# Kernel optimization log

Measured on AMD Instinct MI355X. Metric: run time of the kernel, lower is better.

Reference implementation:

```python
import jax, jax.numpy as jnp
import numpy as np

B, C, F, W, H, E = 2, 8, 256, 512, 8, 4
HD = F // H

def mc_linear(x, w):
    # per-channel linear over features: (b,c,f,w) x (c,g,f) -> (b,c,g,w)
    return jnp.einsum('bcfw,cgf->bcgw', x, w)

def conv2d(x, k, b, ph, pw, groups=1):
    y = jax.lax.conv_general_dilated(x, k, (1, 1), ((ph, ph), (pw, pw)),
                                     dimension_numbers=('NCHW', 'OIHW', 'NCHW'),
                                     feature_group_count=groups)
    return y + b[None, :, None, None]

def mc_ln(x, g, b, eps=1e-5):
    # MultichannelLayerNorm: layernorm over features axis (dim 2), per-channel affine
    m = jnp.mean(x, axis=2, keepdims=True)
    v = jnp.var(x, axis=2, keepdims=True)
    return (x - m) * jax.lax.rsqrt(v + eps) * g[None, :, :, None] + b[None, :, :, None]

def sq_relu(x):
    return jnp.square(jax.nn.relu(x))

def rope(x):
    # x: (b,c,H,n,d); interleaved rotary (lucidrains rotary_embedding_torch)
    n, d = x.shape[-2], x.shape[-1]
    inv = 1.0 / (10000.0 ** (jnp.arange(0, d, 2, dtype=jnp.float32) / d))
    fr = jnp.arange(n, dtype=jnp.float32)[:, None] * inv[None, :]
    cos = jnp.repeat(jnp.cos(fr), 2, axis=-1)
    sin = jnp.repeat(jnp.sin(fr), 2, axis=-1)
    x2 = x.reshape(x.shape[:-1] + (d // 2, 2))
    xr = jnp.stack((-x2[..., 1], x2[..., 0]), axis=-1).reshape(x.shape)
    return x * cos + xr * sin

def mc_attn(x, mem, Wq, Kq, bq, Wk, Kk, bk, Wv, Kv, bv, Wo):
    b, c, f, w = x.shape
    def proj(t, Wl, Kc, bc):
        y = conv2d(mc_linear(t, Wl), Kc, bc, 0, 1)               # (b,c,f,w)
        y = y.transpose(0, 1, 3, 2).reshape(b, c, w, H, HD)
        return y.transpose(0, 1, 3, 2, 4)                        # (b,c,H,w,hd)
    q = rope(proj(x, Wq, Kq, bq))
    k = rope(proj(mem, Wk, Kk, bk))
    v = proj(mem, Wv, Kv, bv)
    # NOTE: original divides by sqrt(h) where h == features, not head_dim
    qk = jnp.einsum('bchnd,bchmd->bchnm', q, k) / jnp.sqrt(jnp.float32(f))
    a = jnp.einsum('bchnm,bchmd->bchnd', jax.nn.softmax(qk, axis=-1), v)
    a = a.transpose(0, 1, 3, 2, 4).reshape(b, c, w, f).transpose(0, 1, 3, 2)
    return mc_linear(a, Wo)

def _forward(x, skip, Wq, Kq, bq, Wk, Kk, bk, Wv, Kv, bv, Wo,
             norm_g, norm_b, c1a_w, c1a_b, c1b_w, c1b_b, c2_w, c2_b, w3, w4):
    att = lambda i, t, m: mc_attn(t, m, Wq[i], Kq[i], bq[i], Wk[i], Kk[i], bk[i],
                                  Wv[i], Kv[i], bv[i], Wo[i])
    h = x  # embed is Identity since channels == out_channels; dropout in eval mode
    z = mc_ln(h, norm_g[0], norm_b[0])
    h = h + att(0, z, z) + att(1, z, skip)
    z = mc_ln(h, norm_g[1], norm_b[1])
    za = sq_relu(conv2d(z, c1a_w, c1a_b, 5, 0, groups=C))   # FrameConv k=11 depthwise
    zb = conv2d(z, c1b_w, c1b_b, 3, 0, groups=C)            # FrameConv k=7 depthwise
    z = conv2d(mc_ln(za + zb, norm_g[2], norm_b[2]), c2_w, c2_b, 3, 0, groups=C)
    h = h + z
    z4 = mc_ln(h, norm_g[3], norm_b[3])
    h = h + att(2, z4, z4)
    h = h + att(3, mc_ln(h, norm_g[4], norm_b[4]), skip)
    z = mc_linear(sq_relu(mc_linear(mc_ln(h, norm_g[5], norm_b[5]), w3)), w4)
    h = h + z
    return jnp.concatenate((x, h), axis=1)

def setup_inputs():
    key = jax.random.key(0)
    ks = jax.random.split(key, 16)
    s = 0.02
    r = lambda k, shp: jax.random.normal(k, shp, dtype=jnp.float32) * s
    return dict(
        x=jax.random.normal(ks[0], (B, C, F, W), dtype=jnp.float32),
        skip=jax.random.normal(ks[1], (B, C, F, W), dtype=jnp.float32),
        Wq=r(ks[2], (4, C, F, F)), Kq=r(ks[3], (4, C, C, 1, 3)), bq=jnp.zeros((4, C), jnp.float32),
        Wk=r(ks[4], (4, C, F, F)), Kk=r(ks[5], (4, C, C, 1, 3)), bk=jnp.zeros((4, C), jnp.float32),
        Wv=r(ks[6], (4, C, F, F)), Kv=r(ks[7], (4, C, C, 1, 3)), bv=jnp.zeros((4, C), jnp.float32),
        Wo=r(ks[8], (4, C, F, F)),
        norm_g=jnp.ones((6, C, F), jnp.float32), norm_b=jnp.zeros((6, C, F), jnp.float32),
        c1a_w=r(ks[9], (C, 1, 11, 1)), c1a_b=jnp.zeros((C,), jnp.float32),
        c1b_w=r(ks[10], (C, 1, 7, 1)), c1b_b=jnp.zeros((C,), jnp.float32),
        c2_w=r(ks[11], (C, 1, 7, 1)), c2_b=jnp.zeros((C,), jnp.float32),
        w3=r(ks[12], (C, E, F)), w4=r(ks[13], (C, F, E)),
    )

def reference(x, skip, Wq, Kq, bq, Wk, Kk, bk, Wv, Kv, bv, Wo,
              norm_g, norm_b, c1a_w, c1a_b, c1b_w, c1b_b, c2_w, c2_b, w3, w4):
    return _forward(x, skip, Wq, Kq, bq, Wk, Kk, bk, Wv, Kv, bv, Wo,
                    norm_g, norm_b, c1a_w, c1a_b, c1b_w, c1b_b, c2_w, c2_b, w3, w4)
```

## Files before the change

### kernel.cpp

```cpp
#include <hip/hip_runtime.h>

#define B_ 2
#define C_ 8
#define F_ 256
#define W_ 512
#define H_ 8
#define FW_ (F_*W_)
#define CFW_ (C_*FW_)
#define OBS_ (2*CFW_)

typedef unsigned short u16;

__device__ __forceinline__ u16 f2bf(float f){
  unsigned u = __float_as_uint(f);
  u += 0x7fffu + ((u>>16)&1u);
  return (u16)(u>>16);
}
__device__ __forceinline__ float bf2f(u16 u){
  return __uint_as_float((unsigned)u<<16);
}

typedef __attribute__((ext_vector_type(8))) short bf16x8;
typedef __attribute__((ext_vector_type(4))) float f32x4;

__global__ __launch_bounds__(256)
void init_out(const float* __restrict__ x, float* __restrict__ out){
  int i = blockIdx.x*256 + threadIdx.x;
  int b = i >> 20;
  int r = i & (CFW_-1);
  float v = x[i];
  out[(size_t)b*OBS_ + r] = v;
  out[(size_t)b*OBS_ + CFW_ + r] = v;
}

__global__ void put_val(float* o, float v){ o[0] = v; }

__global__ __launch_bounds__(256)
void cvt5(const float* __restrict__ s0, const float* __restrict__ s1,
          const float* __restrict__ s2, const float* __restrict__ s3,
          const float* __restrict__ s4,
          u16* __restrict__ d0, u16* __restrict__ d1, u16* __restrict__ d2,
          u16* __restrict__ d3, u16* __restrict__ d4){
  int which = blockIdx.y;
  const float* s = which==0 ? s0 : which==1 ? s1 : which==2 ? s2 : which==3 ? s3 : s4;
  u16* d        = which==0 ? d0 : which==1 ? d1 : which==2 ? d2 : which==3 ? d3 : d4;
  int i = (blockIdx.x*256 + threadIdx.x)*4;
  float4 v = *(const float4*)(s + i);
  ushort4 o;
  o.x = f2bf(v.x); o.y = f2bf(v.y); o.z = f2bf(v.z); o.w = f2bf(v.w);
  *(ushort4*)(d + i) = o;
}

template<int BF16OUT>
__global__ __launch_bounds__(256)
void ln32(const float* __restrict__ X, long xbs, void* __restrict__ Yv, long ybs,
          const float* __restrict__ g, const float* __restrict__ bta){
  int wl = threadIdx.x & 31, fs = threadIdx.x >> 5;
  int w = blockIdx.x*32 + wl;
  int c = blockIdx.y;
  int b = blockIdx.z;
  const float* xb = X + (size_t)b*xbs + (size_t)c*FW_ + w;
  float v[32];
  float sum = 0.f, sq = 0.f;
  #pragma unroll
  for (int i = 0; i < 32; ++i){
    v[i] = xb[(size_t)(fs*32 + i)*W_];
    sum += v[i]; sq += v[i]*v[i];
  }
  __shared__ float Ss[8][32], Sq[8][32], Mu[32], Rs[32];
  Ss[fs][wl] = sum; Sq[fs][wl] = sq;
  __syncthreads();
  if (fs == 0){
    float s = 0.f, q = 0.f;
    #pragma unroll
    for (int j = 0; j < 8; ++j){ s += Ss[j][wl]; q += Sq[j][wl]; }
    float mu = s * (1.f/256.f);
    float var = q * (1.f/256.f) - mu*mu;
    Mu[wl] = mu; Rs[wl] = rsqrtf(var + 1e-5f);
  }
  __syncthreads();
  float mu = Mu[wl], rs = Rs[wl];
  if (BF16OUT){
    u16* yb = (u16*)Yv + (size_t)b*ybs + (size_t)c*FW_ + w;
    #pragma unroll
    for (int i = 0; i < 32; ++i){
      int f = fs*32 + i;
      yb[(size_t)f*W_] = f2bf((v[i] - mu)*rs*g[c*F_ + f] + bta[c*F_ + f]);
    }
  } else {
    float* yb = (float*)Yv + (size_t)b*ybs + (size_t)c*FW_ + w;
    #pragma unroll
    for (int i = 0; i < 32; ++i){
      int f = fs*32 + i;
      yb[(size_t)f*W_] = (v[i] - mu)*rs*g[c*F_ + f] + bta[c*F_ + f];
    }
  }
}

__global__ __launch_bounds__(256)
void gemm_qkv_b(const u16* __restrict__ wqb, const u16* __restrict__ wkb,
                const u16* __restrict__ wvb,
                const u16* __restrict__ srcq, const u16* __restrict__ srckv,
                u16* __restrict__ T){
  int zid = blockIdx.z;
  int proj = zid >> 4;
  int bc = zid & 15; int b = bc >> 3, c = bc & 7;
  const u16* src = (proj == 0) ? srcq : srckv;
  const u16* Wm  = (proj == 0) ? wqb : (proj == 1 ? wkb : wvb);
  const u16* Ax = src + (size_t)b*CFW_ + (size_t)c*FW_;
  const u16* Bw = Wm + (size_t)c*F_*F_;
  u16* Yb = T + (size_t)proj*2*CFW_ + (size_t)b*CFW_ + (size_t)c*FW_;

  int w0 = blockIdx.x * 64;
  int g0 = blockIdx.y * 64;
  int t = threadIdx.x, lane = t & 63, wv_ = t >> 6;
  int gq = lane >> 4, c16 = lane & 15;
  int wm = w0 + wv_*16 + c16;
  const f32x4 zero4 = {0.f,0.f,0.f,0.f};
  f32x4 acc[4] = {zero4, zero4, zero4, zero4};

  for (int k0 = 0; k0 < F_; k0 += 32){
    union { bf16x8 v8; u16 u[8]; } af;
    #pragma unroll
    for (int j = 0; j < 8; ++j)
      af.u[j] = Ax[(size_t)(k0 + 8*gq + j)*W_ + wm];
    #pragma unroll
    for (int nf = 0; nf < 4; ++nf){
      bf16x8 bfr = *(const bf16x8*)(Bw + (size_t)(g0 + nf*16 + c16)*F_ + k0 + 8*gq);
      acc[nf] = __builtin_amdgcn_mfma_f32_16x16x32_bf16(af.v8, bfr, acc[nf], 0, 0, 0);
    }
  }
  int wout = w0 + wv_*16 + 4*gq;
  #pragma unroll
  for (int nf = 0; nf < 4; ++nf){
    ushort4 o;
    o.x = f2bf(acc[nf][0]); o.y = f2bf(acc[nf][1]);
    o.z = f2bf(acc[nf][2]); o.w = f2bf(acc[nf][3]);
    *(ushort4*)(Yb + (size_t)(g0 + nf*16 + c16)*W_ + wout) = o;
  }
}

__global__ __launch_bounds__(256)
void gemm_wo_b(const u16* __restrict__ wob, const u16* __restrict__ A,
               float* __restrict__ Y){
  int bc = blockIdx.z; int b = bc >> 3, c = bc & 7;
  const u16* Ax = A + (size_t)b*CFW_ + (size_t)c*FW_;
  const u16* Bw = wob + (size_t)c*F_*F_;
  float* Yb = Y + (size_t)b*OBS_ + (size_t)c*FW_;
  int w0 = blockIdx.x * 64;
  int g0 = blockIdx.y * 64;
  int t = threadIdx.x, lane = t & 63, wv_ = t >> 6;
  int gq = lane >> 4, c16 = lane & 15;
  int wm = w0 + wv_*16 + c16;
  const f32x4 zero4 = {0.f,0.f,0.f,0.f};
  f32x4 acc[4] = {zero4, zero4, zero4, zero4};

  for (int k0 = 0; k0 < F_; k0 += 32){
    union { bf16x8 v8; u16 u[8]; } af;
    #pragma unroll
    for (int j = 0; j < 8; ++j)
      af.u[j] = Ax[(size_t)(k0 + 8*gq + j)*W_ + wm];
    #pragma unroll
    for (int nf = 0; nf < 4; ++nf){
      bf16x8 bfr = *(const bf16x8*)(Bw + (size_t)(g0 + nf*16 + c16)*F_ + k0 + 8*gq);
      acc[nf] = __builtin_amdgcn_mfma_f32_16x16x32_bf16(af.v8, bfr, acc[nf], 0, 0, 0);
    }
  }
  int wout = w0 + wv_*16 + 4*gq;
  #pragma unroll
  for (int nf = 0; nf < 4; ++nf){
    float* y = Yb + (size_t)(g0 + nf*16 + c16)*W_ + wout;
    float4 o = *(float4*)y;
    o.x += acc[nf][0]; o.y += acc[nf][1]; o.z += acc[nf][2]; o.w += acc[nf][3];
    *(float4*)y = o;
  }
}

__global__ __launch_bounds__(256)
void conv_rope_lds(const u16* __restrict__ T,
                   const float* __restrict__ Kq3, const float* __restrict__ bq,
                   const float* __restrict__ Kk3, const float* __restrict__ bk,
                   const float* __restrict__ Kv3, const float* __restrict__ bv,
                   u16* __restrict__ Q, u16* __restrict__ K,
                   u16* __restrict__ V){
  __shared__ float Tin[16][514];
  __shared__ float Kc[192];
  int bx = blockIdx.x;
  int jf = bx & 127;
  int b  = (bx >> 7) & 1;
  int p  = bx >> 8;
  const float* K3   = p==0 ? Kq3 : (p==1 ? Kk3 : Kv3);
  const float* bias = p==0 ? bq  : (p==1 ? bk  : bv);
  const u16* Tb = T + (size_t)p*2*CFW_ + (size_t)b*CFW_;
  u16* O = (p==0 ? Q : (p==1 ? K : V)) + (size_t)b*CFW_;
  int f0 = jf*2;
  int t = threadIdx.x;

  if (t < 192) Kc[t] = K3[t];
  if (t < 16){ Tin[t][0] = 0.f; Tin[t][513] = 0.f; }
  for (int li = t; li < 16*128; li += 256){
    int row = li >> 7;
    int c4  = li & 127;
    int ci = row >> 1, fsel = row & 1;
    ushort4 v4 = *(const ushort4*)(Tb + ((size_t)ci*F_ + f0 + fsel)*W_ + c4*4);
    float* dst = &Tin[row][1 + c4*4];
    dst[0] = bf2f(v4.x); dst[1] = bf2f(v4.y);
    dst[2] = bf2f(v4.z); dst[3] = bf2f(v4.w);
  }
  __syncthreads();

  int co = t >> 5;
  int wg = t & 31;
  int wbase = wg*16;
  float bs = bias[co];
  float a0[16], a1[16];
  #pragma unroll
  for (int i = 0; i < 16; ++i){ a0[i] = bs; a1[i] = bs; }
  #pragma unroll
  for (int ci = 0; ci < 8; ++ci){
    const float* r0 = &Tin[ci*2+0][1 + wbase];
    const float* r1 = &Tin[ci*2+1][1 + wbase];
    float k0 = Kc[(co*8+ci)*3+0], k1 = Kc[(co*8+ci)*3+1], k2 = Kc[(co*8+ci)*3+2];
    #pragma unroll
    for (int i = 0; i < 16; ++i){
      a0[i] += k0*r0[i-1] + k1*r0[i] + k2*r0[i+1];
      a1[i] += k0*r1[i-1] + k1*r1[i] + k2*r1[i+1];
    }
  }
  size_t obase = ((size_t)co*F_ + f0)*W_ + wbase;
  if (p < 2){
    int j = jf & 15;
    float inv = exp2f(-(float)j * 0.83048202372184f);
    float sv, cv, dsn, dcs;
    sincosf((float)wbase * inv, &sv, &cv);
    sincosf(inv, &dsn, &dcs);
    float scale = (p == 0) ? 0.0625f : 1.f;
    u16 o0[16], o1[16];
    #pragma unroll
    for (int i = 0; i < 16; ++i){
      o0[i] = f2bf((a0[i]*cv - a1[i]*sv)*scale);
      o1[i] = f2bf((a1[i]*cv + a0[i]*sv)*scale);
      float cn = cv*dcs - sv*dsn;
      sv = sv*dcs + cv*dsn;
      cv = cn;
    }
    #pragma unroll
    for (int q4 = 0; q4 < 4; ++q4){
      *(ushort4*)(O + obase + q4*4)      = make_ushort4(o0[q4*4],o0[q4*4+1],o0[q4*4+2],o0[q4*4+3]);
      *(ushort4*)(O + obase + W_ + q4*4) = make_ushort4(o1[q4*4],o1[q4*4+1],o1[q4*4+2],o1[q4*4+3]);
    }
  } else {
    #pragma unroll
    for (int q4 = 0; q4 < 4; ++q4){
      ushort4 p0, p1;
      p0.x = f2bf(a0[q4*4+0]); p0.y = f2bf(a0[q4*4+1]);
      p0.z = f2bf(a0[q4*4+2]); p0.w = f2bf(a0[q4*4+3]);
      p1.x = f2bf(a1[q4*4+0]); p1.y = f2bf(a1[q4*4+1]);
      p1.z = f2bf(a1[q4*4+2]); p1.w = f2bf(a1[q4*4+3]);
      *(ushort4*)(O + obase + q4*4)      = p0;
      *(ushort4*)(O + obase + W_ + q4*4) = p1;
    }
  }
}

__global__ __launch_bounds__(512)
void attn_mfma_b(const u16* __restrict__ q, const u16* __restrict__ k,
                 const u16* __restrict__ v, u16* __restrict__ a){
  extern __shared__ __align__(16) unsigned char smem_dyn[];
  u16* ks = (u16*)smem_dyn;
  u16* vs = ks + 512*40;
  u16* ps = vs + 32*520;
  int bx = blockIdx.x;
  int b = bx >> 6;
  int ch = bx & 63;
  int h = ch & 7, c = ch >> 3;
  size_t base = (size_t)b*CFW_ + ((size_t)c*F_ + h*32)*W_;
  int t = threadIdx.x;
  int lane = t & 63, wv = t >> 6;
  int g = lane >> 4, c16 = lane & 15;

  int q0 = blockIdx.y*128 + wv*16;
  union { bf16x8 v8; u16 u[8]; } aq;
  #pragma unroll
  for (int j = 0; j < 8; ++j)
    aq.u[j] = q[base + (size_t)(8*g + j)*W_ + q0 + c16];

  for (int d = 0; d < 32; ++d)
    ks[t*40 + d] = k[base + (size_t)d*W_ + t];
  {
    int m8 = (t & 63)*8;
    #pragma unroll
    for (int it = 0; it < 4; ++it){
      int d = (t >> 6) + it*8;
      *(uint4*)(vs + (size_t)d*520 + m8) = *(const uint4*)(v + base + (size_t)d*W_ + m8);
    }
  }
  __syncthreads();

  u16* pw = ps + (size_t)wv*16*136;

  float mrun[4] = {-3e38f,-3e38f,-3e38f,-3e38f};
  float lrun[4] = {0.f,0.f,0.f,0.f};
  const f32x4 zero4 = {0.f,0.f,0.f,0.f};
  f32x4 outacc[2] = {zero4, zero4};

  for (int kt = 0; kt < 4; ++kt){
    f32x4 sv[8];
    #pragma unroll
    for (int mi = 0; mi < 8; ++mi){
      int m0 = kt*128 + mi*16;
      bf16x8 kb8 = *(const bf16x8*)(ks + (size_t)(m0 + c16)*40 + 8*g);
      sv[mi] = __builtin_amdgcn_mfma_f32_16x16x32_bf16(aq.v8, kb8, zero4, 0, 0, 0);
    }
    float pmax[4];
    #pragma unroll
    for (int r = 0; r < 4; ++r){
      float m = sv[0][r];
      #pragma unroll
      for (int mi = 1; mi < 8; ++mi) m = fmaxf(m, sv[mi][r]);
      pmax[r] = m;
    }
    #pragma unroll
    for (int mask = 1; mask <= 8; mask <<= 1){
      #pragma unroll
      for (int r = 0; r < 4; ++r)
        pmax[r] = fmaxf(pmax[r], __shfl_xor(pmax[r], mask));
    }
    float corr[4];
    #pragma unroll
    for (int r = 0; r < 4; ++r){
      float mn = fmaxf(mrun[r], pmax[r]);
      corr[r] = __expf(mrun[r] - mn);
      mrun[r] = mn;
      lrun[r] *= corr[r];
    }
    #pragma unroll
    for (int mi = 0; mi < 8; ++mi){
      #pragma unroll
      for (int r = 0; r < 4; ++r){
        float p = __expf(sv[mi][r] - mrun[r]);
        lrun[r] += p;
        pw[(size_t)(4*g + r)*136 + mi*16 + c16] = f2bf(p);
      }
    }
    f32x4 cv = {corr[0], corr[1], corr[2], corr[3]};
    outacc[0] *= cv;
    outacc[1] *= cv;
    #pragma unroll
    for (int mc = 0; mc < 4; ++mc){
      bf16x8 pa  = *(const bf16x8*)(pw + (size_t)c16*136 + mc*32 + 8*g);
      bf16x8 vb0 = *(const bf16x8*)(vs + (size_t)c16*520      + kt*128 + mc*32 + 8*g);
      bf16x8 vb1 = *(const bf16x8*)(vs + (size_t)(16+c16)*520 + kt*128 + mc*32 + 8*g);
      outacc[0] = __builtin_amdgcn_mfma_f32_16x16x32_bf16(pa, vb0, outacc[0], 0, 0, 0);
      outacc[1] = __builtin_amdgcn_mfma_f32_16x16x32_bf16(pa, vb1, outacc[1], 0, 0, 0);
    }
  }
  float L[4];
  #pragma unroll
  for (int r = 0; r < 4; ++r){
    float s = lrun[r];
    #pragma unroll
    for (int mask = 1; mask <= 8; mask <<= 1) s += __shfl_xor(s, mask);
    L[r] = s;
  }
  #pragma unroll
  for (int dt = 0; dt < 2; ++dt){
    ushort4 o;
    o.x = f2bf(outacc[dt][0] / L[0]);
    o.y = f2bf(outacc[dt][1] / L[1]);
    o.z = f2bf(outacc[dt][2] / L[2]);
    o.w = f2bf(outacc[dt][3] / L[3]);
    *(ushort4*)(a + base + (size_t)(dt*16 + c16)*W_ + q0 + 4*g) = o;
  }
}

__global__ __launch_bounds__(256)
void dw_fuse_b(const float* __restrict__ Z, long zbs,
               const float* __restrict__ k11, const float* __restrict__ b11,
               const float* __restrict__ k7,  const float* __restrict__ b7,
               float* __restrict__ S, long sbs){
  int w = blockIdx.x*256 + threadIdx.x;
  int f = blockIdx.y;
  int bc = blockIdx.z; int b = bc >> 3, c = bc & 7;
  const float* zb = Z + (size_t)b*zbs + (size_t)c*FW_;
  float a = b11[c];
  #pragma unroll
  for (int i = 0; i < 11; ++i){
    int ff = f - 5 + i;
    if (ff >= 0 && ff < F_) a += k11[c*11 + i]*zb[(size_t)ff*W_ + w];
  }
  float bb = b7[c];
  #pragma unroll
  for (int i = 0; i < 7; ++i){
    int ff = f - 3 + i;
    if (ff >= 0 && ff < F_) bb += k7[c*7 + i]*zb[(size_t)ff*W_ + w];
  }
  float ra = a > 0.f ? a*a : 0.f;
  S[(size_t)b*sbs + ((size_t)c*F_ + f)*W_ + w] = ra + bb;
}

__global__ __launch_bounds__(256)
void conv7_add_b(const float* __restrict__ T, long tbs,
                 const float* __restrict__ k7, const float* __restrict__ b7,
                 float* __restrict__ Hp, long hbs){
  int w = blockIdx.x*256 + threadIdx.x;
  int f = blockIdx.y;
  int bc = blockIdx.z; int b = bc >> 3, c = bc & 7;
  const float* tb = T + (size_t)b*tbs + (size_t)c*FW_;
  float acc = b7[c];
  #pragma unroll
  for (int i = 0; i < 7; ++i){
    int ff = f - 3 + i;
    if (ff >= 0 && ff < F_) acc += k7[c*7 + i]*tb[(size_t)ff*W_ + w];
  }
  Hp[(size_t)b*hbs + ((size_t)c*F_ + f)*W_ + w] += acc;
}

__global__ __launch_bounds__(256)
void ff_b2(const float* __restrict__ Z, long zbs,
           const float* __restrict__ w3, const float* __restrict__ w4,
           float* __restrict__ Hp, long hbs){
  int wl = threadIdx.x & 63, fs = threadIdx.x >> 6;
  int w = blockIdx.x*64 + wl;
  int c = blockIdx.y;
  int b = blockIdx.z;
  const float* zb = Z + (size_t)b*zbs + (size_t)c*FW_ + w;
  float u[4] = {0.f,0.f,0.f,0.f};
  for (int i = 0; i < 64; ++i){
    int f = fs*64 + i;
    float zv = zb[(size_t)f*W_];
    #pragma unroll
    for (int e = 0; e < 4; ++e) u[e] += w3[(c*4 + e)*F_ + f]*zv;
  }
  __shared__ float Us[4][4][64];
  #pragma unroll
  for (int e = 0; e < 4; ++e) Us[fs][e][wl] = u[e];
  __syncthreads();
  float uf[4];
  #pragma unroll
  for (int e = 0; e < 4; ++e){
    float s = Us[0][e][wl] + Us[1][e][wl] + Us[2][e][wl] + Us[3][e][wl];
    float rr = s > 0.f ? s : 0.f;
    uf[e] = rr*rr;
  }
  float* hb = Hp + (size_t)b*hbs + (size_t)c*FW_ + w;
  for (int i = 0; i < 64; ++i){
    int f = fs*64 + i;
    const float* w4r = w4 + (c*F_ + f)*4;
    hb[(size_t)f*W_] += w4r[0]*uf[0] + w4r[1]*uf[1] + w4r[2]*uf[2] + w4r[3]*uf[3];
  }
}

extern "C" void kernel_launch(void* const* d_in, const int* in_sizes, int n_in,
                              void* d_out, int out_size, void* d_ws, size_t ws_size,
                              hipStream_t stream){
  const float* x    = (const float*)d_in[0];
  const float* skip = (const float*)d_in[1];
  const float* Wq   = (const float*)d_in[2];
  const float* Kq   = (const float*)d_in[3];
  const float* bq   = (const float*)d_in[4];
  const float* Wk   = (const float*)d_in[5];
  const float* Kk   = (const float*)d_in[6];
  const float* bk   = (const float*)d_in[7];
  const float* Wv   = (const float*)d_in[8];
  const float* Kv   = (const float*)d_in[9];
  const float* bv   = (const float*)d_in[10];
  const float* Wo   = (const float*)d_in[11];
  const float* ng   = (const float*)d_in[12];
  const float* nb   = (const float*)d_in[13];
  const float* c1aw = (const float*)d_in[14];
  const float* c1ab = (const float*)d_in[15];
  const float* c1bw = (const float*)d_in[16];
  const float* c1bb = (const float*)d_in[17];
  const float* c2w  = (const float*)d_in[18];
  const float* c2b  = (const float*)d_in[19];
  const float* w3   = (const float*)d_in[20];
  const float* w4   = (const float*)d_in[21];

  float* out = (float*)d_out;
  float* hp  = out + CFW_;

  char* wsb = (char*)d_ws;
  u16* WQb  = (u16*)(wsb);
  u16* WKb  = (u16*)(wsb + ((size_t)4  << 20));
  u16* WVb  = (u16*)(wsb + ((size_t)8  << 20));
  u16* WOb  = (u16*)(wsb + ((size_t)12 << 20));
  u16* skb  = (u16*)(wsb + ((size_t)16 << 20));
  u16* zb16 = (u16*)(wsb + ((size_t)20 << 20));
  u16* tqkv = (u16*)(wsb + ((size_t)24 << 20));
  u16* qbB  = (u16*)(wsb + ((size_t)36 << 20));
  u16* kbB  = (u16*)(wsb + ((size_t)40 << 20));
  u16* vbB  = (u16*)(wsb + ((size_t)44 << 20));
  float* zf = (float*)(wsb + ((size_t)48 << 20));
  float* sf = (float*)(wsb + ((size_t)56 << 20));
  u16* ab   = tqkv;

  float code = 0.f;
  if (n_in != 22) code += 20000.f;
  if (out_size != 4194304) code += 80000.f;
  if (ws_size < ((size_t)64 << 20)) code += 160000.f;

  dim3 gPix(2, F_, 16);
  dim3 gGemmQKV(8, 4, 48);
  dim3 gGemmWo(8, 4, 16);
  dim3 gLn(16, 8, 2);
  dim3 gFF(8, 8, 2);
  dim3 gAttn(128, 4);
  const int attn_lds_bytes = (512*40 + 32*520 + 8*16*136) * 2;

  init_out<<<8192, 256, 0, stream>>>(x, out);
  cvt5<<<dim3(2048, 5), 256, 0, stream>>>(Wq, Wk, Wv, Wo, skip,
                                          WQb, WKb, WVb, WOb, skb);

  auto do_attn = [&](int i, const u16* srcq, const u16* srckv){
    size_t wo16 = (size_t)i*C_*F_*F_;
    gemm_qkv_b<<<gGemmQKV, 256, 0, stream>>>(WQb + wo16, WKb + wo16, WVb + wo16,
                                             srcq, srckv, tqkv);
    conv_rope_lds<<<768, 256, 0, stream>>>(
        tqkv, Kq + i*C_*C_*3, bq + i*C_, Kk + i*C_*C_*3, bk + i*C_,
        Kv + i*C_*C_*3, bv + i*C_, qbB, kbB, vbB);
    attn_mfma_b<<<gAttn, 512, attn_lds_bytes, stream>>>(qbB, kbB, vbB, ab);
    gemm_wo_b<<<gGemmWo, 256, 0, stream>>>(WOb + wo16, ab, hp);
  };

  ln32<1><<<gLn, 256, 0, stream>>>(x, CFW_, zb16, CFW_, ng + 0*C_*F_, nb + 0*C_*F_);
  do_attn(0, zb16, zb16);
  do_attn(1, zb16, skb);

  ln32<0><<<gLn, 256, 0, stream>>>(hp, OBS_, zf, CFW_, ng + 1*C_*F_, nb + 1*C_*F_);
  dw_fuse_b<<<gPix, 256, 0, stream>>>(zf, CFW_, c1aw, c1ab, c1bw, c1bb, sf, CFW_);
  ln32<0><<<gLn, 256, 0, stream>>>(sf, CFW_, zf, CFW_, ng + 2*C_*F_, nb + 2*C_*F_);
  conv7_add_b<<<gPix, 256, 0, stream>>>(zf, CFW_, c2w, c2b, hp, OBS_);

  ln32<1><<<gLn, 256, 0, stream>>>(hp, OBS_, zb16, CFW_, ng + 3*C_*F_, nb + 3*C_*F_);
  do_attn(2, zb16, zb16);

  ln32<1><<<gLn, 256, 0, stream>>>(hp, OBS_, zb16, CFW_, ng + 4*C_*F_, nb + 4*C_*F_);
  do_attn(3, zb16, skb);

  ln32<0><<<gLn, 256, 0, stream>>>(hp, OBS_, zf, CFW_, ng + 5*C_*F_, nb + 5*C_*F_);
  ff_b2<<<gFF, 256, 0, stream>>>(zf, CFW_, w3, w4, hp, OBS_);

  if (code != 0.f) put_val<<<1, 1, 0, stream>>>(out, code);
}
```

Measured before the change: 438.4 us.

## Store GEMM A-operands feature-contiguous so MFMA fragments load as one vector

The bf16 activations feeding the QKV and output-projection GEMMs (layernorm output, skip, attention output) are now written in a transposed (w, f) layout. Each lane can then fetch its 8-element MFMA A fragment with a single 16-byte load instead of eight strided 2-byte loads. Skip conversion becomes an LDS-tiled transpose kernel, and layernorm writes ushort4 vectors along f. In exchange, the attention epilogue now does scalar 2-byte scattered stores with a large stride, and the layernorm stores are strided across lanes.

```diff
diff --git a/kernel.cpp b/kernel.cpp
--- a/kernel.cpp
+++ b/kernel.cpp
@@ -36,19 +36,45 @@
 __global__ void put_val(float* o, float v){ o[0] = v; }
 
 __global__ __launch_bounds__(256)
-void cvt5(const float* __restrict__ s0, const float* __restrict__ s1,
+void cvt4(const float* __restrict__ s0, const float* __restrict__ s1,
           const float* __restrict__ s2, const float* __restrict__ s3,
-          const float* __restrict__ s4,
           u16* __restrict__ d0, u16* __restrict__ d1, u16* __restrict__ d2,
-          u16* __restrict__ d3, u16* __restrict__ d4){
+          u16* __restrict__ d3){
   int which = blockIdx.y;
-  const float* s = which==0 ? s0 : which==1 ? s1 : which==2 ? s2 : which==3 ? s3 : s4;
-  u16* d        = which==0 ? d0 : which==1 ? d1 : which==2 ? d2 : which==3 ? d3 : d4;
+  const float* s = which==0 ? s0 : which==1 ? s1 : which==2 ? s2 : s3;
+  u16* d        = which==0 ? d0 : which==1 ? d1 : which==2 ? d2 : d3;
   int i = (blockIdx.x*256 + threadIdx.x)*4;
   float4 v = *(const float4*)(s + i);
   ushort4 o;
   o.x = f2bf(v.x); o.y = f2bf(v.y); o.z = f2bf(v.z); o.w = f2bf(v.w);
   *(ushort4*)(d + i) = o;
+}
+
+__global__ __launch_bounds__(256)
+void cvtT(const float* __restrict__ src, u16* __restrict__ dst){
+  __shared__ float Tin[64][65];
+  int w0 = blockIdx.x*64, f0 = blockIdx.y*64;
+  int bc = blockIdx.z; int b = bc >> 3, c = bc & 7;
+  const float* s = src + (size_t)b*CFW_ + (size_t)c*FW_;
+  int t = threadIdx.x;
+  int r16 = t >> 4, c4 = (t & 15)*4;
+  #pragma unroll
+  for (int pass = 0; pass < 4; ++pass){
+    int f = r16 + pass*16;
+    float4 v = *(const float4*)(s + (size_t)(f0+f)*W_ + w0 + c4);
+    Tin[f][c4+0] = v.x; Tin[f][c4+1] = v.y;
+    Tin[f][c4+2] = v.z; Tin[f][c4+3] = v.w;
+  }
+  __syncthreads();
+  u16* d = dst + (size_t)b*CFW_ + (size_t)c*FW_;
+  #pragma unroll
+  for (int pass = 0; pass < 4; ++pass){
+    int w = r16 + pass*16;
+    ushort4 o;
+    o.x = f2bf(Tin[c4+0][w]); o.y = f2bf(Tin[c4+1][w]);
+    o.z = f2bf(Tin[c4+2][w]); o.w = f2bf(Tin[c4+3][w]);
+    *(ushort4*)(d + (size_t)(w0+w)*F_ + f0 + c4) = o;
+  }
 }
 
 template<int BF16OUT>
@@ -81,11 +107,16 @@
   __syncthreads();
   float mu = Mu[wl], rs = Rs[wl];
   if (BF16OUT){
-    u16* yb = (u16*)Yv + (size_t)b*ybs + (size_t)c*FW_ + w;
-    #pragma unroll
-    for (int i = 0; i < 32; ++i){
-      int f = fs*32 + i;
-      yb[(size_t)f*W_] = f2bf((v[i] - mu)*rs*g[c*F_ + f] + bta[c*F_ + f]);
+    u16* yb = (u16*)Yv + (size_t)b*ybs + ((size_t)c*W_ + w)*F_ + fs*32;
+    #pragma unroll
+    for (int i4 = 0; i4 < 8; ++i4){
+      ushort4 o;
+      int f = fs*32 + i4*4;
+      o.x = f2bf((v[i4*4+0] - mu)*rs*g[c*F_ + f+0] + bta[c*F_ + f+0]);
+      o.y = f2bf((v[i4*4+1] - mu)*rs*g[c*F_ + f+1] + bta[c*F_ + f+1]);
+      o.z = f2bf((v[i4*4+2] - mu)*rs*g[c*F_ + f+2] + bta[c*F_ + f+2]);
+      o.w = f2bf((v[i4*4+3] - mu)*rs*g[c*F_ + f+3] + bta[c*F_ + f+3]);
+      *(ushort4*)(yb + i4*4) = o;
     }
   } else {
     float* yb = (float*)Yv + (size_t)b*ybs + (size_t)c*FW_ + w;
@@ -107,7 +138,7 @@
   int bc = zid & 15; int b = bc >> 3, c = bc & 7;
   const u16* src = (proj == 0) ? srcq : srckv;
   const u16* Wm  = (proj == 0) ? wqb : (proj == 1 ? wkb : wvb);
-  const u16* Ax = src + (size_t)b*CFW_ + (size_t)c*FW_;
+  const u16* AxT = src + (size_t)b*CFW_ + (size_t)c*FW_;
   const u16* Bw = Wm + (size_t)c*F_*F_;
   u16* Yb = T + (size_t)proj*2*CFW_ + (size_t)b*CFW_ + (size_t)c*FW_;
 
@@ -120,14 +151,11 @@
   f32x4 acc[4] = {zero4, zero4, zero4, zero4};
 
   for (int k0 = 0; k0 < F_; k0 += 32){
-    union { bf16x8 v8; u16 u[8]; } af;
-    #pragma unroll
-    for (int j = 0; j < 8; ++j)
-      af.u[j] = Ax[(size_t)(k0 + 8*gq + j)*W_ + wm];
+    bf16x8 af = *(const bf16x8*)(AxT + (size_t)wm*F_ + k0 + 8*gq);
     #pragma unroll
     for (int nf = 0; nf < 4; ++nf){
       bf16x8 bfr = *(const bf16x8*)(Bw + (size_t)(g0 + nf*16 + c16)*F_ + k0 + 8*gq);
-      acc[nf] = __builtin_amdgcn_mfma_f32_16x16x32_bf16(af.v8, bfr, acc[nf], 0, 0, 0);
+      acc[nf] = __builtin_amdgcn_mfma_f32_16x16x32_bf16(af, bfr, acc[nf], 0, 0, 0);
     }
   }
   int wout = w0 + wv_*16 + 4*gq;
@@ -144,7 +172,7 @@
 void gemm_wo_b(const u16* __restrict__ wob, const u16* __restrict__ A,
                float* __restrict__ Y){
   int bc = blockIdx.z; int b = bc >> 3, c = bc & 7;
-  const u16* Ax = A + (size_t)b*CFW_ + (size_t)c*FW_;
+  const u16* AxT = A + (size_t)b*CFW_ + (size_t)c*FW_;
   const u16* Bw = wob + (size_t)c*F_*F_;
   float* Yb = Y + (size_t)b*OBS_ + (size_t)c*FW_;
   int w0 = blockIdx.x * 64;
@@ -156,14 +184,11 @@
   f32x4 acc[4] = {zero4, zero4, zero4, zero4};
 
   for (int k0 = 0; k0 < F_; k0 += 32){
-    union { bf16x8 v8; u16 u[8]; } af;
-    #pragma unroll
-    for (int j = 0; j < 8; ++j)
-      af.u[j] = Ax[(size_t)(k0 + 8*gq + j)*W_ + wm];
+    bf16x8 af = *(const bf16x8*)(AxT + (size_t)wm*F_ + k0 + 8*gq);
     #pragma unroll
     for (int nf = 0; nf < 4; ++nf){
       bf16x8 bfr = *(const bf16x8*)(Bw + (size_t)(g0 + nf*16 + c16)*F_ + k0 + 8*gq);
-      acc[nf] = __builtin_amdgcn_mfma_f32_16x16x32_bf16(af.v8, bfr, acc[nf], 0, 0, 0);
+      acc[nf] = __builtin_amdgcn_mfma_f32_16x16x32_bf16(af, bfr, acc[nf], 0, 0, 0);
     }
   }
   int wout = w0 + wv_*16 + 4*gq;
@@ -265,7 +290,7 @@
 
 __global__ __launch_bounds__(512)
 void attn_mfma_b(const u16* __restrict__ q, const u16* __restrict__ k,
-                 const u16* __restrict__ v, u16* __restrict__ a){
+                 const u16* __restrict__ v, u16* __restrict__ aT){
   extern __shared__ __align__(16) unsigned char smem_dyn[];
   u16* ks = (u16*)smem_dyn;
   u16* vs = ks + 512*40;
@@ -363,14 +388,13 @@
     for (int mask = 1; mask <= 8; mask <<= 1) s += __shfl_xor(s, mask);
     L[r] = s;
   }
+  size_t tbase = (size_t)b*CFW_ + (size_t)c*FW_;
   #pragma unroll
   for (int dt = 0; dt < 2; ++dt){
-    ushort4 o;
-    o.x = f2bf(outacc[dt][0] / L[0]);
-    o.y = f2bf(outacc[dt][1] / L[1]);
-    o.z = f2bf(outacc[dt][2] / L[2]);
-    o.w = f2bf(outacc[dt][3] / L[3]);
-    *(ushort4*)(a + base + (size_t)(dt*16 + c16)*W_ + q0 + 4*g) = o;
+    #pragma unroll
+    for (int r = 0; r < 4; ++r)
+      aT[tbase + (size_t)(q0 + 4*g + r)*F_ + h*32 + dt*16 + c16]
+        = f2bf(outacc[dt][r] / L[r]);
   }
 }
 
@@ -485,15 +509,15 @@
   u16* WKb  = (u16*)(wsb + ((size_t)4  << 20));
   u16* WVb  = (u16*)(wsb + ((size_t)8  << 20));
   u16* WOb  = (u16*)(wsb + ((size_t)12 << 20));
-  u16* skb  = (u16*)(wsb + ((size_t)16 << 20));
-  u16* zb16 = (u16*)(wsb + ((size_t)20 << 20));
+  u16* skT  = (u16*)(wsb + ((size_t)16 << 20));
+  u16* zT   = (u16*)(wsb + ((size_t)20 << 20));
   u16* tqkv = (u16*)(wsb + ((size_t)24 << 20));
   u16* qbB  = (u16*)(wsb + ((size_t)36 << 20));
   u16* kbB  = (u16*)(wsb + ((size_t)40 << 20));
   u16* vbB  = (u16*)(wsb + ((size_t)44 << 20));
   float* zf = (float*)(wsb + ((size_t)48 << 20));
   float* sf = (float*)(wsb + ((size_t)56 << 20));
-  u16* ab   = tqkv;
+  u16* aT   = tqkv;
 
   float code = 0.f;
   if (n_in != 22) code += 20000.f;
@@ -506,11 +530,12 @@
   dim3 gLn(16, 8, 2);
   dim3 gFF(8, 8, 2);
   dim3 gAttn(128, 4);
+  dim3 gCvtT(8, 4, 16);
   const int attn_lds_bytes = (512*40 + 32*520 + 8*16*136) * 2;
 
   init_out<<<8192, 256, 0, stream>>>(x, out);
-  cvt5<<<dim3(2048, 5), 256, 0, stream>>>(Wq, Wk, Wv, Wo, skip,
-                                          WQb, WKb, WVb, WOb, skb);
+  cvt4<<<dim3(2048, 4), 256, 0, stream>>>(Wq, Wk, Wv, Wo, WQb, WKb, WVb, WOb);
+  cvtT<<<gCvtT, 256, 0, stream>>>(skip, skT);
 
   auto do_attn = [&](int i, const u16* srcq, const u16* srckv){
     size_t wo16 = (size_t)i*C_*F_*F_;
@@ -519,24 +544,24 @@
     conv_rope_lds<<<768, 256, 0, stream>>>(
         tqkv, Kq + i*C_*C_*3, bq + i*C_, Kk + i*C_*C_*3, bk + i*C_,
         Kv + i*C_*C_*3, bv + i*C_, qbB, kbB, vbB);
-    attn_mfma_b<<<gAttn, 512, attn_lds_bytes, stream>>>(qbB, kbB, vbB, ab);
-    gemm_wo_b<<<gGemmWo, 256, 0, stream>>>(WOb + wo16, ab, hp);
+    attn_mfma_b<<<gAttn, 512, attn_lds_bytes, stream>>>(qbB, kbB, vbB, aT);
+    gemm_wo_b<<<gGemmWo, 256, 0, stream>>>(WOb + wo16, aT, hp);
   };
 
-  ln32<1><<<gLn, 256, 0, stream>>>(x, CFW_, zb16, CFW_, ng + 0*C_*F_, nb + 0*C_*F_);
-  do_attn(0, zb16, zb16);
-  do_attn(1, zb16, skb);
+  ln32<1><<<gLn, 256, 0, stream>>>(x, CFW_, zT, CFW_, ng + 0*C_*F_, nb + 0*C_*F_);
+  do_attn(0, zT, zT);
+  do_attn(1, zT, skT);
 
   ln32<0><<<gLn, 256, 0, stream>>>(hp, OBS_, zf, CFW_, ng + 1*C_*F_, nb + 1*C_*F_);
   dw_fuse_b<<<gPix, 256, 0, stream>>>(zf, CFW_, c1aw, c1ab, c1bw, c1bb, sf, CFW_);
   ln32<0><<<gLn, 256, 0, stream>>>(sf, CFW_, zf, CFW_, ng + 2*C_*F_, nb + 2*C_*F_);
   conv7_add_b<<<gPix, 256, 0, stream>>>(zf, CFW_, c2w, c2b, hp, OBS_);
 
-  ln32<1><<<gLn, 256, 0, stream>>>(hp, OBS_, zb16, CFW_, ng + 3*C_*F_, nb + 3*C_*F_);
-  do_attn(2, zb16, zb16);
-
-  ln32<1><<<gLn, 256, 0, stream>>>(hp, OBS_, zb16, CFW_, ng + 4*C_*F_, nb + 4*C_*F_);
-  do_attn(3, zb16, skb);
+  ln32<1><<<gLn, 256, 0, stream>>>(hp, OBS_, zT, CFW_, ng + 3*C_*F_, nb + 3*C_*F_);
+  do_attn(2, zT, zT);
+
+  ln32<1><<<gLn, 256, 0, stream>>>(hp, OBS_, zT, CFW_, ng + 4*C_*F_, nb + 4*C_*F_);
+  do_attn(3, zT, skT);
 
   ln32<0><<<gLn, 256, 0, stream>>>(hp, OBS_, zf, CFW_, ng + 5*C_*F_, nb + 5*C_*F_);
   ff_b2<<<gFF, 256, 0, stream>>>(zf, CFW_, w3, w4, hp, OBS_);
```

Result: slower. 452.2 us (+3.2%).
